# Kernel tuning notes

Measured on AMD Instinct MI355X. Metric: run time of the kernel, lower is better.

The kernel has to match this reference:

```python
import jax, jax.numpy as jnp
import numpy as np

N, H, W, DIM = 8, 32, 32, 768
HEAD_DIM = 64
NUM_HEADS = DIM // HEAD_DIM
KERNEL = (7, 7)
ROT_DIM = HEAD_DIM // 2  # 32
POS_DIM = 2
THETA = 10000.0
LN_EPS = 1e-5


def setup_inputs() -> dict:
    key = jax.random.key(0)
    k_x, k_qkv, k_out = jax.random.split(key, 3)
    S = H * W
    x = jax.random.normal(k_x, (N, S, DIM), dtype=jnp.float32)
    # 2D grid positions, same for every batch element
    grid = jnp.stack(jnp.meshgrid(jnp.arange(H), jnp.arange(W), indexing='ij'), axis=-1)
    pos = jnp.broadcast_to(grid.reshape(1, S, 2), (N, S, 2)).astype(jnp.int32)
    padding_mask = jnp.ones((N, S), dtype=bool)
    ln_g = jnp.ones((DIM,), dtype=jnp.float32)
    ln_b = jnp.zeros((DIM,), dtype=jnp.float32)
    w_qkv = jax.random.normal(k_qkv, (DIM, 3 * DIM), dtype=jnp.float32) * 0.02
    b_qkv = jnp.zeros((3 * DIM,), dtype=jnp.float32)
    w_out = jax.random.normal(k_out, (DIM, DIM), dtype=jnp.float32) * 0.02
    b_out = jnp.zeros((DIM,), dtype=jnp.float32)
    return {"x": x, "pos": pos, "padding_mask": padding_mask,
            "ln_g": ln_g, "ln_b": ln_b,
            "w_qkv": w_qkv, "b_qkv": b_qkv,
            "w_out": w_out, "b_out": b_out}


def _rope_cos_sin(pos):
    # freqs: theta ** linspace(0, -1, rot_dim // (pos_dim*2) + 1)[:-1] -> 8 freqs
    n_freq = ROT_DIM // (POS_DIM * 2)
    freqs = THETA ** jnp.linspace(0.0, -1.0, n_freq + 1, dtype=jnp.float32)[:-1]
    # pos: [n, s, 2] -> [n, s, 2, n_freq] -> [n, s, 2*n_freq] -> [n, 1, s, 2*n_freq]
    tmp = (pos[..., None].astype(jnp.float32) * freqs).reshape(*pos.shape[:-1], -1)[:, None]
    return jnp.cos(tmp), jnp.sin(tmp)


def _apply_rotary(x, cos, sin):
    d = cos.shape[-1]  # 16
    x1, x2, x3 = x[..., :d], x[..., d:2 * d], x[..., 2 * d:]
    y1 = x1 * cos - x2 * sin
    y2 = x2 * cos + x1 * sin
    return jnp.concatenate((y1.astype(x3.dtype), y2.astype(x3.dtype), x3), axis=-1)


def _attn_mask(pos, padding_mask, kernel_size):
    dh = pos[:, :, None, 0] - pos[:, None, :, 0]  # [n, s, s]
    dw = pos[:, :, None, 1] - pos[:, None, :, 1]
    kh, kw = kernel_size
    m = ((dh <= kh // 2) & (dh > -((kh + 1) // 2))
         & (dw <= kw // 2) & (dw > -((kw + 1) // 2)))
    m = m & (padding_mask[:, None, :] & padding_mask[:, :, None])
    return m[:, None]  # [n, 1, s, s]


def reference(x, pos, padding_mask, ln_g, ln_b, w_qkv, b_qkv, w_out, b_out):
    n, s, dim = x.shape
    skip = x
    # LayerNorm
    mu = jnp.mean(x, axis=-1, keepdims=True)
    var = jnp.mean(jnp.square(x - mu), axis=-1, keepdims=True)
    xn = (x - mu) * jax.lax.rsqrt(var + LN_EPS) * ln_g + ln_b
    # QKV projection; split 'n s (t h d)'
    qkv = xn @ w_qkv + b_qkv                       # [n, s, 3*dim]
    qkv = qkv.reshape(n, s, 3, NUM_HEADS, HEAD_DIM)
    qkv = jnp.transpose(qkv, (2, 0, 3, 1, 4))      # [3, n, h, s, d]
    q, k, v = qkv[0], qkv[1], qkv[2]
    # RoPE on first half of head dim
    cos, sin = _rope_cos_sin(pos)
    q = _apply_rotary(q, cos, sin)
    k = _apply_rotary(k, cos, sin)
    # Local 2D-window masked SDPA
    mask = _attn_mask(pos, padding_mask, KERNEL)   # [n, 1, s, s]
    scale = 1.0 / jnp.sqrt(jnp.asarray(HEAD_DIM, dtype=q.dtype))
    scores = jnp.einsum('nhqd,nhkd->nhqk', q, k) * scale
    scores = jnp.where(mask, scores, jnp.asarray(-1e30, dtype=scores.dtype))
    attn = jax.nn.softmax(scores, axis=-1)
    o = jnp.einsum('nhqk,nhkd->nhqd', attn, v)     # [n, h, s, d]
    o = jnp.transpose(o, (0, 2, 1, 3)).reshape(n, s, dim)
    return o @ w_out + b_out + skip
```

## Files before the change

kernel.cpp:

```cpp
#include <hip/hip_runtime.h>


typedef unsigned short u16;
typedef unsigned int   u32;
typedef __attribute__((ext_vector_type(8))) short v8s;
typedef __attribute__((ext_vector_type(4))) float v4f;
typedef __attribute__((ext_vector_type(4))) unsigned short v4us;

#define MFMA16(a,b,c) __builtin_amdgcn_mfma_f32_16x16x32_bf16((a),(b),(c),0,0,0)

__device__ __forceinline__ u16 f2bf(float f){
  union { float f; u32 u; } v; v.f = f;
  u32 u = v.u;
  u32 r = u + 0x7FFFu + ((u >> 16) & 1u);
  return (u16)(r >> 16);
}
__device__ __forceinline__ float bf2f(u16 h){
  union { u32 u; float f; } v; v.u = ((u32)h) << 16;
  return v.f;
}
__device__ __forceinline__ void gll16(const void* g, void* l){
  __builtin_amdgcn_global_load_lds((const __attribute__((address_space(1))) void*)g,
                                   (__attribute__((address_space(3))) void*)l, 16, 0, 0);
}
__device__ __forceinline__ v8s ld8(const u16* p){ return *(const v8s*)p; }
__device__ __forceinline__ void st8(u16* p, v8s v){ *(v8s*)p = v; }

__global__ __launch_bounds__(256)
void jet_prep(const float* __restrict__ x, const float* __restrict__ g,
              const float* __restrict__ b, u16* __restrict__ xn,
              const float* __restrict__ w0, u16* __restrict__ t0,
              const float* __restrict__ w1, u16* __restrict__ t1)
{
  __shared__ float sh[32 * 33];
  const int bid = blockIdx.x, t = threadIdx.x;
  if (bid < 8192){
    const float* xr = x + (size_t)bid * 768;
    float a0 = xr[t], a1 = xr[t + 256], a2 = xr[t + 512];
    float s  = a0 + a1 + a2;
    float ss = a0*a0 + a1*a1 + a2*a2;
    #pragma unroll
    for (int o = 1; o < 64; o <<= 1){ s += __shfl_xor(s, o); ss += __shfl_xor(ss, o); }
    const int wv = t >> 6, lane = t & 63;
    if (lane == 0){ sh[wv] = s; sh[4 + wv] = ss; }
    __syncthreads();
    s  = sh[0] + sh[1] + sh[2] + sh[3];
    ss = sh[4] + sh[5] + sh[6] + sh[7];
    const float mu = s * (1.0f / 768.0f);
    const float var = ss * (1.0f / 768.0f) - mu * mu;
    const float rs = rsqrtf(var + 1e-5f);
    u16* o = xn + (size_t)bid * 768;
    o[t]       = f2bf((a0 - mu) * rs * g[t]       + b[t]);
    o[t + 256] = f2bf((a1 - mu) * rs * g[t + 256] + b[t + 256]);
    o[t + 512] = f2bf((a2 - mu) * rs * g[t + 512] + b[t + 512]);
  } else {
    const float* in; u16* out; int C, bx, by;
    if (bid < 8192 + 1728){
      const int tb = bid - 8192; in = w0; out = t0; C = 2304; bx = tb % 72; by = tb / 72;
    } else {
      const int tb = bid - 8192 - 1728; in = w1; out = t1; C = 768; bx = tb % 24; by = tb / 24;
    }
    float (*tile)[33] = (float(*)[33])sh;
    const int x0 = bx << 5, y0 = by << 5;
    const int tx = t & 31, ty = t >> 5;
    #pragma unroll
    for (int i = 0; i < 32; i += 8)
      tile[ty + i][tx] = in[(size_t)(y0 + ty + i) * C + x0 + tx];
    __syncthreads();
    #pragma unroll
    for (int i = 0; i < 32; i += 8)
      out[(size_t)(x0 + ty + i) * 768 + y0 + tx] = f2bf(tile[tx][ty + i]);
  }
}

template<int MODE>
__global__ __launch_bounds__(256, 4)
void jet_gemm(const u16* __restrict__ A, const u16* __restrict__ Bt,
              const float* __restrict__ bias, int K,
              u16* __restrict__ qbuf, u16* __restrict__ kbuf, u16* __restrict__ vbuf,
              const float* __restrict__ skip, float* __restrict__ outp)
{
  __shared__ u16 As[2][128 * 32];
  __shared__ u16 Bs[2][128 * 32];
  const int tid = threadIdx.x;
  const int lane = tid & 63, wv = tid >> 6;
  const int wm = wv >> 1, wn = wv & 1;
  const int row0 = blockIdx.x * 128, col0 = blockIdx.y * 128;
  const int lq = lane & 15, lk = lane >> 4;

  v4f acc[4][4] = {};

  auto stage = [&](int bsel, int kt){
    const int k0 = kt * 32;
    #pragma unroll
    for (int i = 0; i < 2; ++i){
      const int lin = i * 256 + tid;
      const int r = lin >> 2, c = lin & 3;
      const int sc = c ^ ((r >> 1) & 3);
      gll16(A  + (size_t)(row0 + r) * K + k0 + (sc << 3), (void*)&As[bsel][lin << 3]);
      gll16(Bt + (size_t)(col0 + r) * K + k0 + (sc << 3), (void*)&Bs[bsel][lin << 3]);
    }
  };

  stage(0, 0);
  __syncthreads();
  const int KT = K >> 5;
  for (int kt = 0; kt < KT; ++kt){
    const int cur = kt & 1;
    if (kt + 1 < KT) stage(cur ^ 1, kt + 1);
    v8s af[4], bf[4];
    #pragma unroll
    for (int m = 0; m < 4; ++m){
      const int row_ = wm*64 + m*16 + lq;
      af[m] = ld8(&As[cur][row_*32 + ((lk ^ ((row_ >> 1) & 3)) << 3)]);
    }
    #pragma unroll
    for (int n = 0; n < 4; ++n){
      const int row_ = wn*64 + n*16 + lq;
      bf[n] = ld8(&Bs[cur][row_*32 + ((lk ^ ((row_ >> 1) & 3)) << 3)]);
    }
    #pragma unroll
    for (int m = 0; m < 4; ++m)
      #pragma unroll
      for (int n = 0; n < 4; ++n)
        acc[m][n] = MFMA16(af[m], bf[n], acc[m][n]);
    __syncthreads();
  }

  if (MODE == 0){
    const int colw = col0 + wn * 64;
    const int which = colw / 768;
    const int cm = colw - which * 768;
    const int hh = cm >> 6;
    float bb[4];
    #pragma unroll
    for (int n = 0; n < 4; ++n) bb[n] = bias[colw + n * 16 + lq];

    if (which == 2){
      #pragma unroll
      for (int m = 0; m < 4; ++m){
        const int rbase = row0 + wm * 64 + m * 16 + lk * 4;
        const int img = rbase >> 10, s = rbase & 1023;
        u16* vp = vbuf + (size_t)(img * 12 + hh) * 64 * 1024;
        #pragma unroll
        for (int n = 0; n < 4; ++n){
          const int d = n * 16 + lq;
          v4us pk;
          #pragma unroll
          for (int r = 0; r < 4; ++r) pk[r] = f2bf(acc[m][n][r] + bb[n]);
          *(v4us*)&vp[(size_t)d * 1024 + s] = pk;
        }
      }
    } else {
      u16* dst0 = (which == 0) ? qbuf : kbuf;
      const float freq = __expf(-(float)(lq & 7) * 1.1512925464970229f);
      #pragma unroll
      for (int m = 0; m < 4; ++m){
        const int rbase = row0 + wm * 64 + m * 16 + lk * 4;
        const int img = rbase >> 10, sb = rbase & 1023;
        u16* dst = dst0 + ((size_t)(img * 12 + hh) * 1024 + sb) * 64;
        #pragma unroll
        for (int r = 0; r < 4; ++r){
          const int s = sb + r;
          const float coord = (float)((lq < 8) ? (s >> 5) : (s & 31));
          float sn, cs;
          __sincosf(coord * freq, &sn, &cs);
          const float x1 = acc[m][0][r] + bb[0];
          const float x2 = acc[m][1][r] + bb[1];
          u16* dr = dst + (size_t)r * 64;
          dr[lq]      = f2bf(x1 * cs - x2 * sn);
          dr[16 + lq] = f2bf(x2 * cs + x1 * sn);
          dr[32 + lq] = f2bf(acc[m][2][r] + bb[2]);
          dr[48 + lq] = f2bf(acc[m][3][r] + bb[3]);
        }
      }
    }
  } else {
    #pragma unroll
    for (int m = 0; m < 4; ++m){
      const int rbase = row0 + wm*64 + m*16 + lk*4;
      #pragma unroll
      for (int n = 0; n < 4; ++n){
        const int col = col0 + wn*64 + n*16 + lq;
        const float bb = bias[col];
        const size_t o = (size_t)rbase * 768 + col;
        #pragma unroll
        for (int r = 0; r < 4; ++r)
          outp[o + (size_t)r * 768] = acc[m][n][r] + bb + skip[o + (size_t)r * 768];
      }
    }
  }
}

__global__ __launch_bounds__(64, 4)
void jet_attn(const u16* __restrict__ qbuf, const u16* __restrict__ kbuf,
              const u16* __restrict__ vbuf, u16* __restrict__ obuf)
{
  __shared__ u16 Ps[16][232];

  const int b0 = blockIdx.x;
  const int blk = (b0 & 7) * 768 + (b0 >> 3);
  const int half = blk & 1;
  const int qh = (blk >> 1) & 31;
  const int nh = blk >> 6;
  const int img = nh / 12, hd = nh - img * 12;
  int h0 = qh - 3; h0 = h0 < 0 ? 0 : (h0 > 25 ? 25 : h0);
  const int s0k = h0 * 32;
  const int lane = threadIdx.x;
  const int lq = lane & 15, lk = lane >> 4;

  const u16* kg = kbuf + ((size_t)nh * 1024 + s0k) * 64;
  const u16* vg = vbuf + (size_t)nh * 64 * 1024;

  const u16* qrow = qbuf + ((size_t)nh * 1024 + qh * 32 + half * 16 + lq) * 64;
  const v8s qf0 = ld8(qrow + lk * 8);
  const v8s qf1 = ld8(qrow + 32 + lk * 8);

  float sc[56];
  const int qw = half * 16 + lq;
  #pragma unroll
  for (int tt = 0; tt < 14; ++tt){
    const u16* krow = kg + (size_t)(tt * 16 + lq) * 64;
    const v8s kf0 = ld8(krow + lk * 8);
    const v8s kf1 = ld8(krow + 32 + lk * 8);
    v4f s = {0.f, 0.f, 0.f, 0.f};
    s = MFMA16(kf0, qf0, s);
    s = MFMA16(kf1, qf1, s);
    #pragma unroll
    for (int r = 0; r < 4; ++r){
      const int k = tt * 16 + lk * 4 + r;
      const int dh = qh - (h0 + (k >> 5));
      const int dw = qw - (k & 31);
      const bool ok = (dh <= 3) & (dh >= -3) & (dw <= 3) & (dw >= -3);
      sc[tt * 4 + r] = ok ? s[r] * 0.125f : -1e30f;
    }
  }

  float mx = -1e30f;
  #pragma unroll
  for (int i = 0; i < 56; ++i) mx = fmaxf(mx, sc[i]);
  mx = fmaxf(mx, __shfl_xor(mx, 16));
  mx = fmaxf(mx, __shfl_xor(mx, 32));
  float sum = 0.f;
  #pragma unroll
  for (int i = 0; i < 56; ++i){
    const float e = __expf(sc[i] - mx);
    sc[i] = e; sum += e;
  }
  sum += __shfl_xor(sum, 16);
  sum += __shfl_xor(sum, 32);
  const float inv = 1.0f / sum;

  #pragma unroll
  for (int tt = 0; tt < 14; ++tt){
    v4us pk;
    #pragma unroll
    for (int r = 0; r < 4; ++r) pk[r] = f2bf(sc[tt * 4 + r] * inv);
    *(v4us*)&Ps[lq][tt * 16 + lk * 4] = pk;
  }

  v4f acc[4] = {};
  #pragma unroll
  for (int ks = 0; ks < 7; ++ks){
    const v8s af = ld8(&Ps[lq][ks * 32 + lk * 8]);
    #pragma unroll
    for (int n = 0; n < 4; ++n){
      const v8s bf = ld8(vg + (size_t)(n * 16 + lq) * 1024 + s0k + ks * 32 + lk * 8);
      acc[n] = MFMA16(af, bf, acc[n]);
    }
  }

  u16* dst = obuf + ((size_t)img * 1024 + qh * 32 + half * 16) * 768 + hd * 64;
  #pragma unroll
  for (int n = 0; n < 4; ++n)
    #pragma unroll
    for (int r = 0; r < 4; ++r)
      dst[(size_t)(lk * 4 + r) * 768 + n * 16 + lq] = f2bf(acc[n][r]);
}

extern "C" void kernel_launch(void* const* d_in, const int* in_sizes, int n_in,
                              void* d_out, int out_size, void* d_ws, size_t ws_size,
                              hipStream_t stream)
{
  const float* x     = (const float*)d_in[0];
  const float* ln_g  = (const float*)d_in[3];
  const float* ln_b  = (const float*)d_in[4];
  const float* w_qkv = (const float*)d_in[5];
  const float* b_qkv = (const float*)d_in[6];
  const float* w_out = (const float*)d_in[7];
  const float* b_out = (const float*)d_in[8];
  float* out = (float*)d_out;

  char* ws = (char*)d_ws;
  size_t off = 0;
  auto alloc = [&](size_t n){ size_t o = off; off += (n + 255) & ~(size_t)255; return o; };
  u16* xn    = (u16*)(ws + alloc(8192ull * 768 * 2));
  u16* wqkvT = (u16*)(ws + alloc(2304ull * 768 * 2));
  u16* woutT = (u16*)(ws + alloc(768ull  * 768 * 2));
  u16* q_buf = (u16*)(ws + alloc(96ull * 1024 * 64 * 2));
  u16* k_buf = (u16*)(ws + alloc(96ull * 1024 * 64 * 2));
  u16* v_buf = (u16*)(ws + alloc(96ull * 1024 * 64 * 2));
  u16* o_buf = (u16*)(ws + alloc(8192ull * 768 * 2));

  jet_prep<<<8192 + 1728 + 576, 256, 0, stream>>>(x, ln_g, ln_b, xn, w_qkv, wqkvT, w_out, woutT);
  jet_gemm<0><<<dim3(64, 18), 256, 0, stream>>>(xn, wqkvT, b_qkv, 768,
                                                q_buf, k_buf, v_buf, nullptr, nullptr);
  jet_attn<<<6144, 64, 0, stream>>>(q_buf, k_buf, v_buf, o_buf);
  jet_gemm<1><<<dim3(64, 6), 256, 0, stream>>>(o_buf, woutT, b_out, 768,
                                               nullptr, nullptr, nullptr, x, out);
}
```

Measured before the change: 126.7 us.

## Process a full 32-query row per attention block to reuse K and V fragments

Each single-wave attention block now handles both 16-query halves of an image row instead of one, so every loaded K and V fragment feeds two MFMAs. The grid is halved and the launch bound drops to 2 waves per SIMD. The aim is to halve global K/V traffic and the per-block setup cost. In exchange, register pressure roughly doubles (two 56-element score arrays), and fewer, larger blocks reduce occupancy and latency hiding.

```diff
diff --git a/kernel.cpp b/kernel.cpp
--- a/kernel.cpp
+++ b/kernel.cpp
@@ -192,17 +192,16 @@
   }
 }
 
-__global__ __launch_bounds__(64, 4)
+__global__ __launch_bounds__(64, 2)
 void jet_attn(const u16* __restrict__ qbuf, const u16* __restrict__ kbuf,
               const u16* __restrict__ vbuf, u16* __restrict__ obuf)
 {
-  __shared__ u16 Ps[16][232];
+  __shared__ u16 Ps[32][232];
 
   const int b0 = blockIdx.x;
-  const int blk = (b0 & 7) * 768 + (b0 >> 3);
-  const int half = blk & 1;
-  const int qh = (blk >> 1) & 31;
-  const int nh = blk >> 6;
+  const int blk = (b0 & 7) * 384 + (b0 >> 3);
+  const int qh = blk & 31;
+  const int nh = blk >> 5;
   const int img = nh / 12, hd = nh - img * 12;
   int h0 = qh - 3; h0 = h0 < 0 ? 0 : (h0 > 25 ? 25 : h0);
   const int s0k = h0 * 32;
@@ -212,70 +211,80 @@
   const u16* kg = kbuf + ((size_t)nh * 1024 + s0k) * 64;
   const u16* vg = vbuf + (size_t)nh * 64 * 1024;
 
-  const u16* qrow = qbuf + ((size_t)nh * 1024 + qh * 32 + half * 16 + lq) * 64;
-  const v8s qf0 = ld8(qrow + lk * 8);
-  const v8s qf1 = ld8(qrow + 32 + lk * 8);
-
-  float sc[56];
-  const int qw = half * 16 + lq;
+  const u16* qrow0 = qbuf + ((size_t)nh * 1024 + qh * 32 + lq) * 64;
+  const u16* qrow1 = qrow0 + 16 * 64;
+  const v8s qa0 = ld8(qrow0 + lk * 8), qa1 = ld8(qrow0 + 32 + lk * 8);
+  const v8s qb0 = ld8(qrow1 + lk * 8), qb1 = ld8(qrow1 + 32 + lk * 8);
+
+  float sa[56], sb[56];
   #pragma unroll
   for (int tt = 0; tt < 14; ++tt){
     const u16* krow = kg + (size_t)(tt * 16 + lq) * 64;
     const v8s kf0 = ld8(krow + lk * 8);
     const v8s kf1 = ld8(krow + 32 + lk * 8);
-    v4f s = {0.f, 0.f, 0.f, 0.f};
-    s = MFMA16(kf0, qf0, s);
-    s = MFMA16(kf1, qf1, s);
+    v4f s0 = {0.f, 0.f, 0.f, 0.f}, s1 = {0.f, 0.f, 0.f, 0.f};
+    s0 = MFMA16(kf0, qa0, s0); s0 = MFMA16(kf1, qa1, s0);
+    s1 = MFMA16(kf0, qb0, s1); s1 = MFMA16(kf1, qb1, s1);
     #pragma unroll
     for (int r = 0; r < 4; ++r){
       const int k = tt * 16 + lk * 4 + r;
       const int dh = qh - (h0 + (k >> 5));
-      const int dw = qw - (k & 31);
-      const bool ok = (dh <= 3) & (dh >= -3) & (dw <= 3) & (dw >= -3);
-      sc[tt * 4 + r] = ok ? s[r] * 0.125f : -1e30f;
-    }
-  }
-
-  float mx = -1e30f;
-  #pragma unroll
-  for (int i = 0; i < 56; ++i) mx = fmaxf(mx, sc[i]);
-  mx = fmaxf(mx, __shfl_xor(mx, 16));
-  mx = fmaxf(mx, __shfl_xor(mx, 32));
-  float sum = 0.f;
+      const int kw = k & 31;
+      const bool okh = (dh <= 3) & (dh >= -3);
+      const int dwa = lq - kw, dwb = 16 + lq - kw;
+      sa[tt * 4 + r] = (okh & (dwa <= 3) & (dwa >= -3)) ? s0[r] * 0.125f : -1e30f;
+      sb[tt * 4 + r] = (okh & (dwb <= 3) & (dwb >= -3)) ? s1[r] * 0.125f : -1e30f;
+    }
+  }
+
+  float mxa = -1e30f, mxb = -1e30f;
+  #pragma unroll
+  for (int i = 0; i < 56; ++i){ mxa = fmaxf(mxa, sa[i]); mxb = fmaxf(mxb, sb[i]); }
+  mxa = fmaxf(mxa, __shfl_xor(mxa, 16)); mxa = fmaxf(mxa, __shfl_xor(mxa, 32));
+  mxb = fmaxf(mxb, __shfl_xor(mxb, 16)); mxb = fmaxf(mxb, __shfl_xor(mxb, 32));
+  float suma = 0.f, sumb = 0.f;
   #pragma unroll
   for (int i = 0; i < 56; ++i){
-    const float e = __expf(sc[i] - mx);
-    sc[i] = e; sum += e;
-  }
-  sum += __shfl_xor(sum, 16);
-  sum += __shfl_xor(sum, 32);
-  const float inv = 1.0f / sum;
+    const float ea = __expf(sa[i] - mxa); sa[i] = ea; suma += ea;
+    const float eb = __expf(sb[i] - mxb); sb[i] = eb; sumb += eb;
+  }
+  suma += __shfl_xor(suma, 16); suma += __shfl_xor(suma, 32);
+  sumb += __shfl_xor(sumb, 16); sumb += __shfl_xor(sumb, 32);
+  const float inva = 1.0f / suma, invb = 1.0f / sumb;
 
   #pragma unroll
   for (int tt = 0; tt < 14; ++tt){
-    v4us pk;
-    #pragma unroll
-    for (int r = 0; r < 4; ++r) pk[r] = f2bf(sc[tt * 4 + r] * inv);
-    *(v4us*)&Ps[lq][tt * 16 + lk * 4] = pk;
-  }
-
-  v4f acc[4] = {};
+    v4us pka, pkb;
+    #pragma unroll
+    for (int r = 0; r < 4; ++r){
+      pka[r] = f2bf(sa[tt * 4 + r] * inva);
+      pkb[r] = f2bf(sb[tt * 4 + r] * invb);
+    }
+    *(v4us*)&Ps[lq][tt * 16 + lk * 4]      = pka;
+    *(v4us*)&Ps[16 + lq][tt * 16 + lk * 4] = pkb;
+  }
+
+  v4f accA[4] = {}, accB[4] = {};
   #pragma unroll
   for (int ks = 0; ks < 7; ++ks){
-    const v8s af = ld8(&Ps[lq][ks * 32 + lk * 8]);
+    const v8s pa = ld8(&Ps[lq][ks * 32 + lk * 8]);
+    const v8s pb = ld8(&Ps[16 + lq][ks * 32 + lk * 8]);
     #pragma unroll
     for (int n = 0; n < 4; ++n){
-      const v8s bf = ld8(vg + (size_t)(n * 16 + lq) * 1024 + s0k + ks * 32 + lk * 8);
-      acc[n] = MFMA16(af, bf, acc[n]);
-    }
-  }
-
-  u16* dst = obuf + ((size_t)img * 1024 + qh * 32 + half * 16) * 768 + hd * 64;
+      const v8s vf = ld8(vg + (size_t)(n * 16 + lq) * 1024 + s0k + ks * 32 + lk * 8);
+      accA[n] = MFMA16(pa, vf, accA[n]);
+      accB[n] = MFMA16(pb, vf, accB[n]);
+    }
+  }
+
+  u16* dst = obuf + ((size_t)img * 1024 + qh * 32) * 768 + hd * 64;
   #pragma unroll
   for (int n = 0; n < 4; ++n)
     #pragma unroll
-    for (int r = 0; r < 4; ++r)
-      dst[(size_t)(lk * 4 + r) * 768 + n * 16 + lq] = f2bf(acc[n][r]);
+    for (int r = 0; r < 4; ++r){
+      dst[(size_t)(lk * 4 + r) * 768 + n * 16 + lq]      = f2bf(accA[n][r]);
+      dst[(size_t)(16 + lk * 4 + r) * 768 + n * 16 + lq] = f2bf(accB[n][r]);
+    }
 }
 
 extern "C" void kernel_launch(void* const* d_in, const int* in_sizes, int n_in,
@@ -305,7 +314,7 @@
   jet_prep<<<8192 + 1728 + 576, 256, 0, stream>>>(x, ln_g, ln_b, xn, w_qkv, wqkvT, w_out, woutT);
   jet_gemm<0><<<dim3(64, 18), 256, 0, stream>>>(xn, wqkvT, b_qkv, 768,
                                                 q_buf, k_buf, v_buf, nullptr, nullptr);
-  jet_attn<<<6144, 64, 0, stream>>>(q_buf, k_buf, v_buf, o_buf);
+  jet_attn<<<3072, 64, 0, stream>>>(q_buf, k_buf, v_buf, o_buf);
   jet_gemm<1><<<dim3(64, 6), 256, 0, stream>>>(o_buf, woutT, b_out, 768,
                                                nullptr, nullptr, nullptr, x, out);
 }
```

Result: faster. 113.3 us, median of 2 (-10.6%).
